# Optimization experiments

Hardware: AMD Instinct MI355X
Metric: run time of the kernel (lower is better)

The kernel has to match this reference:

```python
import jax, jax.numpy as jnp
import numpy as np

MODEL_DIM = 256
NUM_HEAD = 8
HEAD_DIM = MODEL_DIM // NUM_HEAD  # 32
ROT_DIM_AXIS = int(0.5 * HEAD_DIM)  # 16 per axis, 32 total rotated channels
LN_EPS = 1e-5
MASK_BIAS = -1e9  # fp32 precision
SCALE = HEAD_DIM ** -0.5
INIT_RANGE = 0.02
N_LAYERS = 6


def _rotate_half(x):
    # interleaved pairs: (d r) with r=2 -> (-x2, x1) re-interleaved
    x = x.reshape(*x.shape[:-1], -1, 2)
    x1, x2 = x[..., 0], x[..., 1]
    return jnp.stack([-x2, x1], axis=-1).reshape(*x.shape[:-2], -1)


def _axial_freqs(seqlen):
    # RotaryEmbedding('lang' freqs) over t = linspace(-1, 1, seqlen)
    inv_freq = 1.0 / (10000.0 ** (jnp.arange(0, ROT_DIM_AXIS, 2, dtype=jnp.float32) / ROT_DIM_AXIS))
    t = jnp.linspace(-1.0, 1.0, seqlen, dtype=jnp.float32)
    f = jnp.repeat(t[:, None] * inv_freq[None, :], 2, axis=-1)  # (s, ROT_DIM_AXIS)
    fh = jnp.broadcast_to(f[:, None, :], (seqlen, seqlen, ROT_DIM_AXIS))
    fw = jnp.broadcast_to(f[None, :, :], (seqlen, seqlen, ROT_DIM_AXIS))
    return jnp.concatenate([fh, fw], axis=-1)  # (s, s, 2*ROT_DIM_AXIS)


def _apply_rotary(freqs, t):
    rot_dim = freqs.shape[-1]
    t_rot, t_pass = t[..., :rot_dim], t[..., rot_dim:]
    t_rot = t_rot * jnp.cos(freqs) + _rotate_half(t_rot) * jnp.sin(freqs)
    return jnp.concatenate([t_rot, t_pass], axis=-1)


def setup_inputs() -> dict:
    key = jax.random.key(0)
    k1, k2, k3, k4 = jax.random.split(key, 4)
    b, s = 2, 128
    pair_act = jax.random.normal(k1, (b, s, s, MODEL_DIM), dtype=jnp.float32)
    pair_mask = jax.random.randint(k2, (b, s, s), 0, 2).astype(bool)  # True = masked
    Wqkv = jax.random.normal(k3, (3 * MODEL_DIM, MODEL_DIM), dtype=jnp.float32) * INIT_RANGE
    Wout = jax.random.normal(k4, (MODEL_DIM, MODEL_DIM), dtype=jnp.float32) * (INIT_RANGE / np.sqrt(2 * N_LAYERS))
    ln_gamma = jnp.ones((MODEL_DIM,), dtype=jnp.float32)
    ln_beta = jnp.zeros((MODEL_DIM,), dtype=jnp.float32)
    return {"pair_act": pair_act, "pair_mask": pair_mask, "ln_gamma": ln_gamma,
            "ln_beta": ln_beta, "Wqkv": Wqkv, "Wout": Wout}


def reference(pair_act, pair_mask, ln_gamma, ln_beta, Wqkv, Wout):
    # orientation == 'per_row': no axis swap
    b, s = pair_act.shape[0], pair_act.shape[1]
    # LayerNorm over model_dim
    mu = jnp.mean(pair_act, axis=-1, keepdims=True)
    var = jnp.var(pair_act, axis=-1, keepdims=True)
    x = (pair_act - mu) * jax.lax.rsqrt(var + LN_EPS) * ln_gamma + ln_beta
    # QKV projection (no bias)
    qkv = jnp.einsum('bxyd,ed->bxye', x, Wqkv)  # (b, s, s, 3*MODEL_DIM)
    q, k, v = jnp.split(qkv, 3, axis=-1)
    # 2D axial rotary on first 2*ROT_DIM_AXIS channels of the feature dim
    freqs = _axial_freqs(s)  # (s, s, 32)
    q = _apply_rotary(freqs, q)
    k = _apply_rotary(freqs, k)
    # multihead attention per row (axis s1 independent)
    q = q.reshape(b, s, s, NUM_HEAD, HEAD_DIM)
    k = k.reshape(b, s, s, NUM_HEAD, HEAD_DIM)
    v = v.reshape(b, s, s, NUM_HEAD, HEAD_DIM)
    scores = jnp.einsum('bxqhd,bxkhd->bxhqk', q, k) * SCALE  # (b, s1, h, s2, s2)
    mask = pair_mask[:, :, None, None, :]  # (b, s1, 1, 1, s2)
    scores = jnp.where(mask, MASK_BIAS, scores)
    attn = jax.nn.softmax(scores, axis=-1)
    out = jnp.einsum('bxhqk,bxkhd->bxqhd', attn, v).reshape(b, s, s, MODEL_DIM)
    return jnp.einsum('bxyd,ed->bxye', out, Wout)
```

## Files before the change

### kernel.cpp

```cpp
#include <hip/hip_runtime.h>
#include <math.h>
#include <stdint.h>

typedef __attribute__((ext_vector_type(8))) short short8;
typedef __attribute__((ext_vector_type(4))) float floatx4;

#define LN_EPS 1e-5f
#define ATT_SCALE 0.17677669529663687f

__device__ __constant__ float INVF[8] = {
    1.0f, 0.31622776601683794f, 0.1f, 0.031622776601683794f,
    0.01f, 0.0031622776601683794f, 0.001f, 0.00031622776601683794f};

__device__ inline unsigned short f2bf(float f) {
    unsigned u = __float_as_uint(f);
    u += 0x7fffu + ((u >> 16) & 1u);
    return (unsigned short)(u >> 16);
}

__device__ inline void gl_lds16(const unsigned short* g, unsigned short* l) {
    __builtin_amdgcn_global_load_lds(
        (const __attribute__((address_space(1))) void*)(uintptr_t)g,
        (__attribute__((address_space(3))) void*)(uintptr_t)l, 16, 0, 0);
}

__global__ __launch_bounds__(256)
void prep_w(const float* __restrict__ wq, const float* __restrict__ wo,
            unsigned short* __restrict__ bq, unsigned short* __restrict__ bo) {
    int g = blockIdx.x * 256 + threadIdx.x;
    const float* src;
    unsigned short* dst;
    if (g < 49152) { src = wq + (size_t)g * 4; dst = bq + (size_t)g * 4; }
    else { int h = g - 49152; src = wo + (size_t)h * 4; dst = bo + (size_t)h * 4; }
    float4 v = *(const float4*)src;
    uint2 o;
    o.x = (unsigned)f2bf(v.x) | ((unsigned)f2bf(v.y) << 16);
    o.y = (unsigned)f2bf(v.z) | ((unsigned)f2bf(v.w) << 16);
    *(uint2*)dst = o;
}

__global__ __launch_bounds__(512, 2)
void fused_kernel(const float* __restrict__ pair_act, const int* __restrict__ mask,
                  const float* __restrict__ gamma, const float* __restrict__ beta,
                  const unsigned short* __restrict__ Wqkv,
                  const unsigned short* __restrict__ Wout,
                  float* __restrict__ out) {
    __shared__ __align__(16) unsigned short S16[16384];
    __shared__ __align__(16) unsigned short Ks[128 * 40];
    __shared__ __align__(16) unsigned short Vt[32 * 136];
    __shared__ __align__(16) unsigned short Qall[8 * 640];

    int bx = blockIdx.x;
    int tid = threadIdx.x;
    int w = tid >> 6, lane = tid & 63, qd = lane >> 4, lo = lane & 15;
    unsigned short* Qscr = Qall + w * 640;

    float tX = -1.0f + (2.0f / 127.0f) * (float)(bx & 127);

    float msel[8];
    #pragma unroll
    for (int nt = 0; nt < 8; ++nt)
        msel[nt] = mask[bx * 128 + nt * 16 + lo] ? 0.0f : 1.0f;

    short8 a_frag[8];
    {
        int rl = tid >> 2, q0 = tid & 3;
        const float* src = pair_act + ((size_t)(bx * 128 + rl)) * 256 + q0 * 4;
        float4 v[16];
        float s = 0.f;
        #pragma unroll
        for (int u = 0; u < 16; ++u) {
            v[u] = *(const float4*)(src + u * 16);
            s += v[u].x + v[u].y + v[u].z + v[u].w;
        }
        s += __shfl_xor(s, 1);
        s += __shfl_xor(s, 2);
        float mean = s * (1.0f / 256.0f);
        float sq = 0.f;
        #pragma unroll
        for (int u = 0; u < 16; ++u) {
            float d0 = v[u].x - mean, d1 = v[u].y - mean;
            float d2 = v[u].z - mean, d3 = v[u].w - mean;
            sq += d0 * d0 + d1 * d1 + d2 * d2 + d3 * d3;
        }
        sq += __shfl_xor(sq, 1);
        sq += __shfl_xor(sq, 2);
        float rs = rsqrtf(sq * (1.0f / 256.0f) + LN_EPS);

        int rw = 16 * w + lo;
        #pragma unroll
        for (int p = 0; p < 2; ++p) {
            #pragma unroll
            for (int ul = 0; ul < 8; ++ul) {
                int u = p * 8 + ul;
                float4 g4 = *(const float4*)(gamma + q0 * 4 + u * 16);
                float4 b4 = *(const float4*)(beta + q0 * 4 + u * 16);
                unsigned e0 = f2bf((v[u].x - mean) * rs * g4.x + b4.x);
                unsigned e1 = f2bf((v[u].y - mean) * rs * g4.y + b4.y);
                unsigned e2 = f2bf((v[u].z - mean) * rs * g4.z + b4.z);
                unsigned e3 = f2bf((v[u].w - mean) * rs * g4.w + b4.w);
                int cw = 2 * ul + (q0 >> 1);
                int ss = (cw & ~7) | ((cw & 7) ^ (rl & 7));
                uint2 pk;
                pk.x = e0 | (e1 << 16);
                pk.y = e2 | (e3 << 16);
                *(uint2*)&S16[rl * 128 + ss * 8 + (q0 & 1) * 4] = pk;
            }
            __syncthreads();
            #pragma unroll
            for (int cp = 0; cp < 4; ++cp) {
                int ci = cp * 4 + qd;
                int ss = (ci & ~7) | ((ci & 7) ^ (rw & 7));
                a_frag[p * 4 + cp] = *(const short8*)&S16[rw * 128 + ss * 8];
            }
            __syncthreads();
        }
    }

    short8 of[8];
    #pragma unroll
    for (int hc = 0; hc < 4; ++hc) {
        unsigned q_pk[4][2], k_pk[4][2], v_pk[4][2];
        #pragma unroll
        for (int part = 0; part < 3; ++part) {
            if (hc != 0 || part != 0) __syncthreads();
            const unsigned short* Wsrc = Wqkv + (size_t)(part * 256 + hc * 64) * 256;
            #pragma unroll
            for (int i = 0; i < 4; ++i) {
                int rbase = i * 16 + w * 2;
                int row = rbase + (lane >> 5);
                int sl = lane & 31;
                int c = (sl & ~7) | ((sl & 7) ^ (row & 7));
                gl_lds16(Wsrc + (size_t)row * 256 + c * 8, S16 + rbase * 256);
            }
            __syncthreads();
            floatx4 acc[4];
            #pragma unroll
            for (int t = 0; t < 4; ++t) acc[t] = (floatx4){0.f, 0.f, 0.f, 0.f};
            #pragma unroll
            for (int cc = 0; cc < 8; ++cc) {
                #pragma unroll
                for (int t = 0; t < 4; ++t) {
                    int rw2 = t * 16 + lo;
                    int ci = cc * 4 + qd;
                    int ss = (ci & ~7) | ((ci & 7) ^ (rw2 & 7));
                    short8 bf = *(const short8*)&S16[rw2 * 256 + ss * 8];
                    acc[t] = __builtin_amdgcn_mfma_f32_16x16x32_bf16(
                        a_frag[cc], bf, acc[t], 0, 0, 0);
                }
            }
            if (hc == 0 && part < 2) {
                #pragma unroll
                for (int t = 0; t < 2; ++t) {
                    int pi = (t * 16 + lo) >> 1;
                    float invf = INVF[pi & 7];
                    float sgn = (lo & 1) ? 1.0f : -1.0f;
                    #pragma unroll
                    for (int r = 0; r < 4; ++r) {
                        int y = 16 * w + qd * 4 + r;
                        float tp = (pi < 8) ? tX
                                            : (-1.0f + (2.0f / 127.0f) * (float)y);
                        float sn, cs;
                        __sincosf(tp * invf, &sn, &cs);
                        float vv = acc[t][r];
                        float pv = __shfl_xor(vv, 1);
                        acc[t][r] = vv * cs + sgn * pv * sn;
                    }
                }
            }
            #pragma unroll
            for (int t = 0; t < 4; ++t) {
                unsigned p0 = (unsigned)f2bf(acc[t][0]) |
                              ((unsigned)f2bf(acc[t][1]) << 16);
                unsigned p1 = (unsigned)f2bf(acc[t][2]) |
                              ((unsigned)f2bf(acc[t][3]) << 16);
                if (part == 0) { q_pk[t][0] = p0; q_pk[t][1] = p1; }
                else if (part == 1) { k_pk[t][0] = p0; k_pk[t][1] = p1; }
                else { v_pk[t][0] = p0; v_pk[t][1] = p1; }
            }
        }

        #pragma unroll
        for (int sub = 0; sub < 2; ++sub) {
            int h = hc * 2 + sub, tt0 = sub * 2;
            __syncthreads();
            #pragma unroll
            for (int tt = 0; tt < 2; ++tt) {
                int t = tt0 + tt;
                int d = tt * 16 + lo;
                #pragma unroll
                for (int r = 0; r < 4; ++r) {
                    unsigned kv = (k_pk[t][r >> 1] >> ((r & 1) * 16)) & 0xffffu;
                    Ks[(16 * w + qd * 4 + r) * 40 + d] = (unsigned short)kv;
                }
                uint2 pv;
                pv.x = v_pk[t][0];
                pv.y = v_pk[t][1];
                *(uint2*)&Vt[d * 136 + 16 * w + qd * 4] = pv;
            }
            __syncthreads();
            #pragma unroll
            for (int tt = 0; tt < 2; ++tt) {
                int t = tt0 + tt;
                #pragma unroll
                for (int r = 0; r < 4; ++r) {
                    unsigned qv = (q_pk[t][r >> 1] >> ((r & 1) * 16)) & 0xffffu;
                    Qscr[(qd * 4 + r) * 40 + tt * 16 + lo] = (unsigned short)qv;
                }
            }
            short8 aq = *(const short8*)&Qscr[lo * 40 + qd * 8];
            float ef[8][4];
            float sums[4] = {0.f, 0.f, 0.f, 0.f};
            #pragma unroll
            for (int nt = 0; nt < 8; ++nt) {
                short8 bk = *(const short8*)&Ks[(nt * 16 + lo) * 40 + qd * 8];
                floatx4 c = (floatx4){0.f, 0.f, 0.f, 0.f};
                c = __builtin_amdgcn_mfma_f32_16x16x32_bf16(aq, bk, c, 0, 0, 0);
                #pragma unroll
                for (int r = 0; r < 4; ++r) {
                    float e = __expf(c[r] * ATT_SCALE) * msel[nt];
                    ef[nt][r] = e;
                    sums[r] += e;
                }
            }
            float inv[4];
            #pragma unroll
            for (int r = 0; r < 4; ++r) {
                float vv = sums[r];
                vv += __shfl_xor(vv, 1);
                vv += __shfl_xor(vv, 2);
                vv += __shfl_xor(vv, 4);
                vv += __shfl_xor(vv, 8);
                inv[r] = 1.0f / vv;
            }
            floatx4 o[2];
            o[0] = (floatx4){0.f, 0.f, 0.f, 0.f};
            o[1] = (floatx4){0.f, 0.f, 0.f, 0.f};
            #pragma unroll
            for (int c2 = 0; c2 < 4; ++c2) {
                #pragma unroll
                for (int half = 0; half < 2; ++half) {
                    int nt = c2 * 2 + half;
                    #pragma unroll
                    for (int r = 0; r < 4; ++r)
                        Qscr[(qd * 4 + r) * 40 + half * 16 + lo] = f2bf(ef[nt][r]);
                }
                short8 pa = *(const short8*)&Qscr[lo * 40 + qd * 8];
                #pragma unroll
                for (int n = 0; n < 2; ++n) {
                    short8 vb =
                        *(const short8*)&Vt[(n * 16 + lo) * 136 + c2 * 32 + qd * 8];
                    o[n] = __builtin_amdgcn_mfma_f32_16x16x32_bf16(pa, vb, o[n],
                                                                   0, 0, 0);
                }
            }
            #pragma unroll
            for (int n = 0; n < 2; ++n)
                #pragma unroll
                for (int r = 0; r < 4; ++r)
                    Qscr[(qd * 4 + r) * 40 + n * 16 + lo] = f2bf(o[n][r] * inv[r]);
            of[h] = *(const short8*)&Qscr[lo * 40 + qd * 8];
        }
    }

    #pragma unroll
    for (int nc = 0; nc < 4; ++nc) {
        __syncthreads();
        const unsigned short* Wsrc = Wout + (size_t)(nc * 64) * 256;
        #pragma unroll
        for (int i = 0; i < 4; ++i) {
            int rbase = i * 16 + w * 2;
            int row = rbase + (lane >> 5);
            int sl = lane & 31;
            int c = (sl & ~7) | ((sl & 7) ^ (row & 7));
            gl_lds16(Wsrc + (size_t)row * 256 + c * 8, S16 + rbase * 256);
        }
        __syncthreads();
        floatx4 acc[4];
        #pragma unroll
        for (int t = 0; t < 4; ++t) acc[t] = (floatx4){0.f, 0.f, 0.f, 0.f};
        #pragma unroll
        for (int cc = 0; cc < 8; ++cc) {
            #pragma unroll
            for (int t = 0; t < 4; ++t) {
                int rw2 = t * 16 + lo;
                int ci = cc * 4 + qd;
                int ss = (ci & ~7) | ((ci & 7) ^ (rw2 & 7));
                short8 bf = *(const short8*)&S16[rw2 * 256 + ss * 8];
                acc[t] = __builtin_amdgcn_mfma_f32_16x16x32_bf16(of[cc], bf,
                                                                 acc[t], 0, 0, 0);
            }
        }
        #pragma unroll
        for (int t = 0; t < 4; ++t)
            #pragma unroll
            for (int r = 0; r < 4; ++r)
                out[(size_t)(bx * 128 + 16 * w + qd * 4 + r) * 256 + nc * 64 +
                    t * 16 + lo] = acc[t][r];
    }
}

extern "C" void kernel_launch(void* const* d_in, const int* in_sizes, int n_in,
                              void* d_out, int out_size, void* d_ws, size_t ws_size,
                              hipStream_t stream) {
    const float* pair_act = (const float*)d_in[0];
    const int* pair_mask = (const int*)d_in[1];
    const float* ln_gamma = (const float*)d_in[2];
    const float* ln_beta = (const float*)d_in[3];
    const float* Wqkv = (const float*)d_in[4];
    const float* Wout = (const float*)d_in[5];
    float* out = (float*)d_out;

    char* ws = (char*)d_ws;
    unsigned short* wqkv_bf = (unsigned short*)ws;
    unsigned short* wout_bf = (unsigned short*)(ws + 393216);

    prep_w<<<256, 256, 0, stream>>>(Wqkv, Wout, wqkv_bf, wout_bf);
    fused_kernel<<<256, 512, 0, stream>>>(pair_act, pair_mask, ln_gamma, ln_beta,
                                          wqkv_bf, wout_bf, out);
}
```

Measured before the change: 137.8 us.

## Double-buffer weight tiles and K/V staging to overlap loads with MFMA

Weight tiles for the QKV and output projections are now double-buffered in LDS. The next tile is issued via global_load_lds before the current tile's MFMAs, with explicit waitcnt and raw barriers in place of __syncthreads. All 12 QKV tiles are computed first and kept in registers. K/V staging for the next head is double-buffered so one barrier per head suffices. This hides global load latency and cuts barriers, at the cost of doubled LDS and many more live registers, which may reduce occupancy below 2 blocks/CU or cause spills.

```diff
diff --git a/kernel.cpp b/kernel.cpp
--- a/kernel.cpp
+++ b/kernel.cpp
@@ -23,6 +23,26 @@
         (const __attribute__((address_space(1))) void*)(uintptr_t)g,
         (__attribute__((address_space(3))) void*)(uintptr_t)l, 16, 0, 0);
 }
+
+__device__ inline void stage_tile(const unsigned short* __restrict__ Wsrc,
+                                  unsigned short* dst, int w, int lane) {
+    #pragma unroll
+    for (int i = 0; i < 4; ++i) {
+        int rbase = i * 16 + w * 2;
+        int row = rbase + (lane >> 5);
+        int sl = lane & 31;
+        int c = (sl & ~7) | ((sl & 7) ^ (row & 7));
+        gl_lds16(Wsrc + (size_t)row * 256 + c * 8, dst + rbase * 256);
+    }
+}
+
+#define VM0() asm volatile("s_waitcnt vmcnt(0)" ::: "memory")
+#define LG0() asm volatile("s_waitcnt lgkmcnt(0)" ::: "memory")
+#define SBAR()                                 \
+    do {                                       \
+        __builtin_amdgcn_s_barrier();          \
+        __builtin_amdgcn_sched_barrier(0);     \
+    } while (0)
 
 __global__ __launch_bounds__(256)
 void prep_w(const float* __restrict__ wq, const float* __restrict__ wo,
@@ -45,9 +65,9 @@
                   const unsigned short* __restrict__ Wqkv,
                   const unsigned short* __restrict__ Wout,
                   float* __restrict__ out) {
-    __shared__ __align__(16) unsigned short S16[16384];
-    __shared__ __align__(16) unsigned short Ks[128 * 40];
-    __shared__ __align__(16) unsigned short Vt[32 * 136];
+    __shared__ __align__(16) unsigned short S16[2][16384];
+    __shared__ __align__(16) unsigned short Ks[2][128 * 40];
+    __shared__ __align__(16) unsigned short Vt[2][32 * 136];
     __shared__ __align__(16) unsigned short Qall[8 * 640];
 
     int bx = blockIdx.x;
@@ -56,6 +76,8 @@
     unsigned short* Qscr = Qall + w * 640;
 
     float tX = -1.0f + (2.0f / 127.0f) * (float)(bx & 127);
+
+    stage_tile(Wqkv, &S16[1][0], w, lane);
 
     float msel[8];
     #pragma unroll
@@ -104,107 +126,126 @@
                 uint2 pk;
                 pk.x = e0 | (e1 << 16);
                 pk.y = e2 | (e3 << 16);
-                *(uint2*)&S16[rl * 128 + ss * 8 + (q0 & 1) * 4] = pk;
+                *(uint2*)&S16[0][rl * 128 + ss * 8 + (q0 & 1) * 4] = pk;
             }
             __syncthreads();
             #pragma unroll
             for (int cp = 0; cp < 4; ++cp) {
                 int ci = cp * 4 + qd;
                 int ss = (ci & ~7) | ((ci & 7) ^ (rw & 7));
-                a_frag[p * 4 + cp] = *(const short8*)&S16[rw * 128 + ss * 8];
+                a_frag[p * 4 + cp] = *(const short8*)&S16[0][rw * 128 + ss * 8];
             }
             __syncthreads();
         }
     }
 
+    unsigned q_pk[4][4][2], k_pk[4][4][2], v_pk[4][4][2];
+    #pragma unroll
+    for (int t = 0; t < 12; ++t) {
+        VM0();
+        SBAR();
+        const unsigned short* nsrc =
+            (t < 11) ? (Wqkv + (size_t)(t + 1) * 64 * 256) : Wout;
+        stage_tile(nsrc, &S16[t & 1][0], w, lane);
+
+        const unsigned short* Sb = &S16[(t + 1) & 1][0];
+        floatx4 acc[4];
+        #pragma unroll
+        for (int tq = 0; tq < 4; ++tq) acc[tq] = (floatx4){0.f, 0.f, 0.f, 0.f};
+        #pragma unroll
+        for (int cc = 0; cc < 8; ++cc) {
+            #pragma unroll
+            for (int tq = 0; tq < 4; ++tq) {
+                int rw2 = tq * 16 + lo;
+                int ci = cc * 4 + qd;
+                int ss = (ci & ~7) | ((ci & 7) ^ (rw2 & 7));
+                short8 bf = *(const short8*)&Sb[rw2 * 256 + ss * 8];
+                acc[tq] = __builtin_amdgcn_mfma_f32_16x16x32_bf16(
+                    a_frag[cc], bf, acc[tq], 0, 0, 0);
+            }
+        }
+        if (t == 0 || t == 4) {
+            #pragma unroll
+            for (int tc = 0; tc < 2; ++tc) {
+                int pi = (tc * 16 + lo) >> 1;
+                float invf = INVF[pi & 7];
+                float sgn = (lo & 1) ? 1.0f : -1.0f;
+                #pragma unroll
+                for (int r = 0; r < 4; ++r) {
+                    int y = 16 * w + qd * 4 + r;
+                    float tp = (pi < 8) ? tX
+                                        : (-1.0f + (2.0f / 127.0f) * (float)y);
+                    float sn, cs;
+                    __sincosf(tp * invf, &sn, &cs);
+                    float vv = acc[tc][r];
+                    float pv = __shfl_xor(vv, 1);
+                    acc[tc][r] = vv * cs + sgn * pv * sn;
+                }
+            }
+        }
+        int part = t >> 2, hc = t & 3;
+        #pragma unroll
+        for (int tq = 0; tq < 4; ++tq) {
+            unsigned p0 = (unsigned)f2bf(acc[tq][0]) |
+                          ((unsigned)f2bf(acc[tq][1]) << 16);
+            unsigned p1 = (unsigned)f2bf(acc[tq][2]) |
+                          ((unsigned)f2bf(acc[tq][3]) << 16);
+            if (part == 0) { q_pk[hc][tq][0] = p0; q_pk[hc][tq][1] = p1; }
+            else if (part == 1) { k_pk[hc][tq][0] = p0; k_pk[hc][tq][1] = p1; }
+            else { v_pk[hc][tq][0] = p0; v_pk[hc][tq][1] = p1; }
+        }
+    }
+
+    {
+        #pragma unroll
+        for (int tt = 0; tt < 2; ++tt) {
+            int tC = tt;
+            int d = tt * 16 + lo;
+            #pragma unroll
+            for (int r = 0; r < 4; ++r) {
+                unsigned kv = (k_pk[0][tC][r >> 1] >> ((r & 1) * 16)) & 0xffffu;
+                Ks[0][(16 * w + qd * 4 + r) * 40 + d] = (unsigned short)kv;
+            }
+            uint2 pv;
+            pv.x = v_pk[0][tC][0];
+            pv.y = v_pk[0][tC][1];
+            *(uint2*)&Vt[0][d * 136 + 16 * w + qd * 4] = pv;
+        }
+    }
+    LG0();
+    SBAR();
+    stage_tile(Wout + (size_t)64 * 256, &S16[0][0], w, lane);
+
     short8 of[8];
     #pragma unroll
-    for (int hc = 0; hc < 4; ++hc) {
-        unsigned q_pk[4][2], k_pk[4][2], v_pk[4][2];
-        #pragma unroll
-        for (int part = 0; part < 3; ++part) {
-            if (hc != 0 || part != 0) __syncthreads();
-            const unsigned short* Wsrc = Wqkv + (size_t)(part * 256 + hc * 64) * 256;
-            #pragma unroll
-            for (int i = 0; i < 4; ++i) {
-                int rbase = i * 16 + w * 2;
-                int row = rbase + (lane >> 5);
-                int sl = lane & 31;
-                int c = (sl & ~7) | ((sl & 7) ^ (row & 7));
-                gl_lds16(Wsrc + (size_t)row * 256 + c * 8, S16 + rbase * 256);
-            }
-            __syncthreads();
-            floatx4 acc[4];
-            #pragma unroll
-            for (int t = 0; t < 4; ++t) acc[t] = (floatx4){0.f, 0.f, 0.f, 0.f};
-            #pragma unroll
-            for (int cc = 0; cc < 8; ++cc) {
-                #pragma unroll
-                for (int t = 0; t < 4; ++t) {
-                    int rw2 = t * 16 + lo;
-                    int ci = cc * 4 + qd;
-                    int ss = (ci & ~7) | ((ci & 7) ^ (rw2 & 7));
-                    short8 bf = *(const short8*)&S16[rw2 * 256 + ss * 8];
-                    acc[t] = __builtin_amdgcn_mfma_f32_16x16x32_bf16(
-                        a_frag[cc], bf, acc[t], 0, 0, 0);
-                }
-            }
-            if (hc == 0 && part < 2) {
-                #pragma unroll
-                for (int t = 0; t < 2; ++t) {
-                    int pi = (t * 16 + lo) >> 1;
-                    float invf = INVF[pi & 7];
-                    float sgn = (lo & 1) ? 1.0f : -1.0f;
-                    #pragma unroll
-                    for (int r = 0; r < 4; ++r) {
-                        int y = 16 * w + qd * 4 + r;
-                        float tp = (pi < 8) ? tX
-                                            : (-1.0f + (2.0f / 127.0f) * (float)y);
-                        float sn, cs;
-                        __sincosf(tp * invf, &sn, &cs);
-                        float vv = acc[t][r];
-                        float pv = __shfl_xor(vv, 1);
-                        acc[t][r] = vv * cs + sgn * pv * sn;
-                    }
-                }
-            }
-            #pragma unroll
-            for (int t = 0; t < 4; ++t) {
-                unsigned p0 = (unsigned)f2bf(acc[t][0]) |
-                              ((unsigned)f2bf(acc[t][1]) << 16);
-                unsigned p1 = (unsigned)f2bf(acc[t][2]) |
-                              ((unsigned)f2bf(acc[t][3]) << 16);
-                if (part == 0) { q_pk[t][0] = p0; q_pk[t][1] = p1; }
-                else if (part == 1) { k_pk[t][0] = p0; k_pk[t][1] = p1; }
-                else { v_pk[t][0] = p0; v_pk[t][1] = p1; }
-            }
-        }
-
-        #pragma unroll
-        for (int sub = 0; sub < 2; ++sub) {
-            int h = hc * 2 + sub, tt0 = sub * 2;
-            __syncthreads();
+    for (int h = 0; h < 8; ++h) {
+        if (h < 7) {
+            int g = h + 1, hcg = g >> 1, tg0 = (g & 1) * 2, kb = g & 1;
             #pragma unroll
             for (int tt = 0; tt < 2; ++tt) {
-                int t = tt0 + tt;
+                int tC = tg0 + tt;
                 int d = tt * 16 + lo;
                 #pragma unroll
                 for (int r = 0; r < 4; ++r) {
-                    unsigned kv = (k_pk[t][r >> 1] >> ((r & 1) * 16)) & 0xffffu;
-                    Ks[(16 * w + qd * 4 + r) * 40 + d] = (unsigned short)kv;
+                    unsigned kv =
+                        (k_pk[hcg][tC][r >> 1] >> ((r & 1) * 16)) & 0xffffu;
+                    Ks[kb][(16 * w + qd * 4 + r) * 40 + d] = (unsigned short)kv;
                 }
                 uint2 pv;
-                pv.x = v_pk[t][0];
-                pv.y = v_pk[t][1];
-                *(uint2*)&Vt[d * 136 + 16 * w + qd * 4] = pv;
-            }
-            __syncthreads();
+                pv.x = v_pk[hcg][tC][0];
+                pv.y = v_pk[hcg][tC][1];
+                *(uint2*)&Vt[kb][d * 136 + 16 * w + qd * 4] = pv;
+            }
+        }
+        {
+            int hch = h >> 1, cb = h & 1;
             #pragma unroll
             for (int tt = 0; tt < 2; ++tt) {
-                int t = tt0 + tt;
+                int tC = (h & 1) * 2 + tt;
                 #pragma unroll
                 for (int r = 0; r < 4; ++r) {
-                    unsigned qv = (q_pk[t][r >> 1] >> ((r & 1) * 16)) & 0xffffu;
+                    unsigned qv =
+                        (q_pk[hch][tC][r >> 1] >> ((r & 1) * 16)) & 0xffffu;
                     Qscr[(qd * 4 + r) * 40 + tt * 16 + lo] = (unsigned short)qv;
                 }
             }
@@ -213,7 +254,7 @@
             float sums[4] = {0.f, 0.f, 0.f, 0.f};
             #pragma unroll
             for (int nt = 0; nt < 8; ++nt) {
-                short8 bk = *(const short8*)&Ks[(nt * 16 + lo) * 40 + qd * 8];
+                short8 bk = *(const short8*)&Ks[cb][(nt * 16 + lo) * 40 + qd * 8];
                 floatx4 c = (floatx4){0.f, 0.f, 0.f, 0.f};
                 c = __builtin_amdgcn_mfma_f32_16x16x32_bf16(aq, bk, c, 0, 0, 0);
                 #pragma unroll
@@ -233,9 +274,9 @@
                 vv += __shfl_xor(vv, 8);
                 inv[r] = 1.0f / vv;
             }
-            floatx4 o[2];
-            o[0] = (floatx4){0.f, 0.f, 0.f, 0.f};
-            o[1] = (floatx4){0.f, 0.f, 0.f, 0.f};
+            floatx4 o2[2];
+            o2[0] = (floatx4){0.f, 0.f, 0.f, 0.f};
+            o2[1] = (floatx4){0.f, 0.f, 0.f, 0.f};
             #pragma unroll
             for (int c2 = 0; c2 < 4; ++c2) {
                 #pragma unroll
@@ -243,60 +284,62 @@
                     int nt = c2 * 2 + half;
                     #pragma unroll
                     for (int r = 0; r < 4; ++r)
-                        Qscr[(qd * 4 + r) * 40 + half * 16 + lo] = f2bf(ef[nt][r]);
+                        Qscr[(qd * 4 + r) * 40 + half * 16 + lo] =
+                            f2bf(ef[nt][r]);
                 }
                 short8 pa = *(const short8*)&Qscr[lo * 40 + qd * 8];
                 #pragma unroll
                 for (int n = 0; n < 2; ++n) {
-                    short8 vb =
-                        *(const short8*)&Vt[(n * 16 + lo) * 136 + c2 * 32 + qd * 8];
-                    o[n] = __builtin_amdgcn_mfma_f32_16x16x32_bf16(pa, vb, o[n],
-                                                                   0, 0, 0);
+                    short8 vb = *(const short8*)&Vt[cb][(n * 16 + lo) * 136 +
+                                                       c2 * 32 + qd * 8];
+                    o2[n] = __builtin_amdgcn_mfma_f32_16x16x32_bf16(pa, vb,
+                                                                    o2[n], 0, 0, 0);
                 }
             }
             #pragma unroll
             for (int n = 0; n < 2; ++n)
                 #pragma unroll
                 for (int r = 0; r < 4; ++r)
-                    Qscr[(qd * 4 + r) * 40 + n * 16 + lo] = f2bf(o[n][r] * inv[r]);
+                    Qscr[(qd * 4 + r) * 40 + n * 16 + lo] =
+                        f2bf(o2[n][r] * inv[r]);
             of[h] = *(const short8*)&Qscr[lo * 40 + qd * 8];
         }
+        LG0();
+        if (h == 7) VM0();
+        SBAR();
     }
 
     #pragma unroll
     for (int nc = 0; nc < 4; ++nc) {
-        __syncthreads();
-        const unsigned short* Wsrc = Wout + (size_t)(nc * 64) * 256;
-        #pragma unroll
-        for (int i = 0; i < 4; ++i) {
-            int rbase = i * 16 + w * 2;
-            int row = rbase + (lane >> 5);
-            int sl = lane & 31;
-            int c = (sl & ~7) | ((sl & 7) ^ (row & 7));
-            gl_lds16(Wsrc + (size_t)row * 256 + c * 8, S16 + rbase * 256);
-        }
-        __syncthreads();
+        if (nc) {
+            VM0();
+            SBAR();
+            if (nc < 3)
+                stage_tile(Wout + (size_t)(nc + 1) * 64 * 256,
+                           &S16[nc & 1][0], w, lane);
+        }
+        const unsigned short* Sb = &S16[(nc + 1) & 1][0];
         floatx4 acc[4];
         #pragma unroll
-        for (int t = 0; t < 4; ++t) acc[t] = (floatx4){0.f, 0.f, 0.f, 0.f};
+        for (int tq = 0; tq < 4; ++tq) acc[tq] = (floatx4){0.f, 0.f, 0.f, 0.f};
         #pragma unroll
         for (int cc = 0; cc < 8; ++cc) {
             #pragma unroll
-            for (int t = 0; t < 4; ++t) {
-                int rw2 = t * 16 + lo;
+            for (int tq = 0; tq < 4; ++tq) {
+                int rw2 = tq * 16 + lo;
                 int ci = cc * 4 + qd;
                 int ss = (ci & ~7) | ((ci & 7) ^ (rw2 & 7));
-                short8 bf = *(const short8*)&S16[rw2 * 256 + ss * 8];
-                acc[t] = __builtin_amdgcn_mfma_f32_16x16x32_bf16(of[cc], bf,
-                                                                 acc[t], 0, 0, 0);
-            }
-        }
-        #pragma unroll
-        for (int t = 0; t < 4; ++t)
+                short8 bf = *(const short8*)&Sb[rw2 * 256 + ss * 8];
+                acc[tq] = __builtin_amdgcn_mfma_f32_16x16x32_bf16(
+                    of[cc], bf, acc[tq], 0, 0, 0);
+            }
+        }
+        #pragma unroll
+        for (int tq = 0; tq < 4; ++tq)
             #pragma unroll
             for (int r = 0; r < 4; ++r)
                 out[(size_t)(bx * 128 + 16 * w + qd * 4 + r) * 256 + nc * 64 +
-                    t * 16 + lo] = acc[t][r];
+                    tq * 16 + lo] = acc[tq][r];
     }
 }
 
```

Measured after the change: 138.3 us. No clear change (+0.4%).
